# Kernel tuning notes

Measured on AMD Instinct MI355X. Metric: run time of the kernel, lower is better.

The kernel has to match this reference:

```python
import jax, jax.numpy as jnp
import numpy as np

E, D_IN, H1, H2 = 10, 784, 256, 64


def setup_inputs() -> dict:
    key = jax.random.key(0)
    ks = jax.random.split(key, 11)
    s = lambda fan_in: 1.0 / np.sqrt(fan_in)
    return {
        "x": jax.random.normal(ks[0], (65536, D_IN), dtype=jnp.float32),
        # stacked expert weights (E experts of Linear layers)
        "W1": jax.random.uniform(ks[1], (E, D_IN, H1), jnp.float32, -s(D_IN), s(D_IN)),
        "b1": jax.random.uniform(ks[2], (E, H1), jnp.float32, -s(D_IN), s(D_IN)),
        "W2": jax.random.uniform(ks[3], (E, H1, H2), jnp.float32, -s(H1), s(H1)),
        "b2": jax.random.uniform(ks[4], (E, H2), jnp.float32, -s(H1), s(H1)),
        "W3": jax.random.uniform(ks[5], (E, H2), jnp.float32, -s(H2), s(H2)),  # [E,64,1] squeezed
        "b3": jax.random.uniform(ks[6], (E,), jnp.float32, -s(H2), s(H2)),
        # gate: 784 -> 256 -> E
        "Wg1": jax.random.uniform(ks[7], (D_IN, H1), jnp.float32, -s(D_IN), s(D_IN)),
        "bg1": jax.random.uniform(ks[8], (H1,), jnp.float32, -s(D_IN), s(D_IN)),
        "Wg2": jax.random.uniform(ks[9], (H1, E), jnp.float32, -s(H1), s(H1)),
        "bg2": jax.random.uniform(ks[10], (E,), jnp.float32, -s(H1), s(H1)),
    }


def reference(x, W1, b1, W2, b2, W3, b3, Wg1, bg1, Wg2, bg2):
    # dense all-experts MLP stack, batched over experts as grouped GEMMs
    h = jax.nn.relu(jnp.einsum("bi,eih->beh", x, W1) + b1)        # [B,E,256]
    h = jax.nn.relu(jnp.einsum("beh,ehk->bek", h, W2) + b2)        # [B,E,64]
    expert_outputs = jnp.einsum("bek,ek->be", h, W3) + b3          # [B,E]
    g = jax.nn.relu(x @ Wg1 + bg1)
    gate_scores = jax.nn.softmax(g @ Wg2 + bg2, axis=-1)           # [B,E]
    output = gate_scores * expert_outputs                          # [B,E]
    return (output, gate_scores, expert_outputs)
```

## Files before the change

kernel.cpp:

```cpp
#include <hip/hip_runtime.h>
#include <hip/hip_bf16.h>
#include <stdint.h>

#define BTOT   65536
#define DIN    784
#define NH1    256
#define NH2    64
#define NEXP   10
#define BM     256
#define NKS1   25

#define SLOT(s)   (lds + (s) * 32768)
#define EXPL_OFF  131072
#define B2S_OFF   141312
#define W3S_OFF   143872
#define B3S_OFF   146432
#define BG2S_OFF  146496
#define LDS_TOTAL 146560

typedef short s16x8  __attribute__((ext_vector_type(8)));
typedef float f32x4  __attribute__((ext_vector_type(4)));
typedef float f32x16 __attribute__((ext_vector_type(16)));

__device__ __forceinline__ short bf16b(float v) {
    __bf16 b = (__bf16)v;
    return __builtin_bit_cast(short, b);
}

__device__ __forceinline__ void g2l16(const void* g, void* l) {
    __builtin_amdgcn_global_load_lds(
        (const __attribute__((address_space(1))) unsigned char*)g,
        (__attribute__((address_space(3))) unsigned char*)l, 16, 0, 0);
}

__global__ void prep_w1(const float* __restrict__ W1, const float* __restrict__ b1,
                        const float* __restrict__ Wg1, const float* __restrict__ bg1,
                        __bf16* __restrict__ dst) {
    int t = blockIdx.x * 256 + threadIdx.x;
    int lane = t & 63;
    int kh = (t >> 6) & 1;
    int nb = (t >> 7) & 7;
    int r  = t >> 10;
    int ks = r % 25, e = r / 25;
    int n  = nb * 32 + (lane & 31);
    int k0 = ks * 32 + kh * 16 + (lane >> 5) * 8;
    const float* src  = (e < NEXP) ? (W1 + (size_t)e * DIN * NH1) : Wg1;
    const float* bias = (e < NEXP) ? (b1 + e * NH1) : bg1;
    s16x8 o;
    #pragma unroll
    for (int j = 0; j < 8; ++j) {
        int k = k0 + j;
        float v = (k < DIN) ? src[(size_t)k * NH1 + n]
                            : ((k == DIN) ? bias[n] : 0.f);
        o[j] = bf16b(v);
    }
    *(s16x8*)((short*)dst + (size_t)t * 8) = o;
}

__global__ void prep_w2(const float* __restrict__ W2, __bf16* __restrict__ dst) {
    int t = blockIdx.x * 256 + threadIdx.x;
    int lane = t & 63;
    int kh = (t >> 6) & 1;
    int ks = (t >> 7) & 7;
    int jb = (t >> 10) & 1;
    int e  = t >> 11;
    int n  = jb * 32 + (lane & 31);
    int k0 = ks * 32 + kh * 16 + (lane >> 5) * 8;
    s16x8 o;
    #pragma unroll
    for (int j = 0; j < 8; ++j)
        o[j] = bf16b(W2[((size_t)e * NH1 + k0 + j) * NH2 + n]);
    *(s16x8*)((short*)dst + (size_t)t * 8) = o;
}

__global__ void prep_wg2(const float* __restrict__ Wg2, __bf16* __restrict__ dst) {
    int t = blockIdx.x * 256 + threadIdx.x;
    if (t >= 1024) return;
    int lane = t & 63;
    int kh = (t >> 6) & 1;
    int ks = t >> 7;
    int n  = lane & 31;
    int k0 = ks * 32 + kh * 16 + (lane >> 5) * 8;
    s16x8 o;
    #pragma unroll
    for (int j = 0; j < 8; ++j)
        o[j] = bf16b((n < NEXP) ? Wg2[(size_t)(k0 + j) * NEXP + n] : 0.f);
    *(s16x8*)((short*)dst + (size_t)t * 8) = o;
}

#define STAGE(S, E, KS) {                                                     \
        const char* xs_ = xtc + ((size_t)(KS) << 14) + tid * 16;              \
        char* xd_ = SLOT(S) + tid * 16;                                       \
        g2l16(xs_, xd_); g2l16(xs_ + 8192, xd_ + 8192);                       \
        const char* ws_ = w1c + (((size_t)(E) * 25 + (KS)) << 14) + tid * 16; \
        char* wd_ = SLOT(S) + 16384 + tid * 16;                               \
        g2l16(ws_, wd_); g2l16(ws_ + 8192, wd_ + 8192); }

#define WSTAGE1(S, KS) {                                                      \
        const char* ws_ = w1c + ((size_t)(KS) << 14) + tid * 16;              \
        char* wd_ = SLOT(S) + 16384 + tid * 16;                               \
        g2l16(ws_, wd_); g2l16(ws_ + 8192, wd_ + 8192); }

#define XLOAD(KS) { if ((KS) < 24 || xkh == 0) {                              \
            _Pragma("unroll") for (int i4 = 0; i4 < 4; ++i4)                  \
                *(float4*)(xf + 4 * i4) =                                     \
                    *(const float4*)(xrp + (KS) * 32 + 4 * i4);               \
        } else { _Pragma("unroll") for (int i4 = 0; i4 < 16; ++i4)            \
                     xf[i4] = 0.f;                                            \
                 xf[0] = 1.f; } }

#define XWRITE(B, KS) { s16x8 l8, h8;                                         \
        _Pragma("unroll") for (int j = 0; j < 8; ++j) {                       \
            l8[j] = bf16b(xf[j]); h8[j] = bf16b(xf[8 + j]); }                 \
        *(s16x8*)(SLOT(B) + xoff)       = l8;                                 \
        *(s16x8*)(SLOT(B) + xoff + 512) = h8;                                 \
        char* xg_ = xtw + ((size_t)(KS) << 14) + xoff;                        \
        *(s16x8*)xg_ = l8; *(s16x8*)(xg_ + 512) = h8; }

#define COMPUTE(S) {                                                          \
        const char* ab = SLOT(S) + mw * 4096 + lane * 16;                     \
        const char* wb = SLOT(S) + 16384 + nw * 8192 + lane * 16;             \
        s16x8 xv[2][2], wv[4][2];                                             \
        _Pragma("unroll") for (int mt = 0; mt < 2; ++mt)                      \
            _Pragma("unroll") for (int kh = 0; kh < 2; ++kh)                  \
                xv[mt][kh] = *(const s16x8*)(ab + (mt * 2 + kh) * 1024);      \
        _Pragma("unroll") for (int nt = 0; nt < 4; ++nt)                      \
            _Pragma("unroll") for (int kh = 0; kh < 2; ++kh)                  \
                wv[nt][kh] = *(const s16x8*)(wb + (nt * 2 + kh) * 1024);      \
        _Pragma("unroll") for (int kh = 0; kh < 2; ++kh)                      \
            _Pragma("unroll") for (int nt = 0; nt < 4; ++nt)                  \
                _Pragma("unroll") for (int mt = 0; mt < 2; ++mt)              \
                    acc[nt][mt] = __builtin_amdgcn_mfma_f32_32x32x16_bf16(    \
                        wv[nt][kh], xv[mt][kh], acc[nt][mt], 0, 0, 0); }

#define RING_SYNC(VN) {                                                       \
        asm volatile("s_waitcnt vmcnt(" #VN ")" ::: "memory");                \
        __builtin_amdgcn_s_barrier();                                         \
        asm volatile("" ::: "memory"); }

#define BODY(S, KS) {                                                         \
        RING_SYNC(8)                                                          \
        COMPUTE(S)                                                            \
        STAGE(((S) + 3) & 3, e, (KS) + 3) }

__global__ void __launch_bounds__(512)
__attribute__((amdgpu_waves_per_eu(2, 2)))
moe_fused(const float* __restrict__ x, __bf16* __restrict__ xt,
          const float* __restrict__ b2g, const float* __restrict__ W3,
          const float* __restrict__ b3, const float* __restrict__ bg2,
          const __bf16* __restrict__ w1t, const __bf16* __restrict__ w2t,
          const __bf16* __restrict__ wg2t, float* __restrict__ out)
{
    extern __shared__ char lds[];
    char*  hb   = lds;
    float* expl = (float*)(lds + EXPL_OFF);
    float* b2s  = (float*)(lds + B2S_OFF);
    float* w3s  = (float*)(lds + W3S_OFF);
    float* b3s  = (float*)(lds + B3S_OFF);
    float* bg2s = (float*)(lds + BG2S_OFF);

    const int tid  = threadIdx.x;
    const int lane = tid & 63;
    const int wave = tid >> 6;
    const int rl   = lane & 31;
    const int hi   = lane >> 5;
    const int mw   = wave >> 1;
    const int nw   = wave & 1;
    const int row0 = blockIdx.x * BM;
    const char* w1c = (const char*)w1t;
    const char* w2c = (const char*)w2t;
    const char* wgc = (const char*)wg2t;
    const char* xtc = (const char*)xt + ((size_t)blockIdx.x * 25 << 14);
    char*       xtw = (char*)xt + ((size_t)blockIdx.x * 25 << 14);

    const int xrow = tid >> 1, xkh = tid & 1;
    const float* xrp = x + (size_t)(row0 + xrow) * DIN + xkh * 16;
    const int xoff = ((xrow >> 5) * 2 + xkh) * 1024 + (xrow & 31) * 16;
    float xf[16];

    for (int i = tid; i < NEXP * NH2; i += 512) { b2s[i] = b2g[i]; w3s[i] = W3[i]; }
    if (tid < NEXP) { b3s[tid] = b3[tid]; bg2s[tid] = bg2[tid]; }
    __syncthreads();

    f32x16 acc[4][2];

    #pragma unroll 1
    for (int e = 0; e <= NEXP; ++e) {
        #pragma unroll
        for (int nt = 0; nt < 4; ++nt)
            #pragma unroll
            for (int mt = 0; mt < 2; ++mt)
                #pragma unroll
                for (int q = 0; q < 16; ++q) acc[nt][mt][q] = 0.f;

        if (e == 0) {
            int cur = 0;
            XLOAD(0)
            WSTAGE1(0, 0)
            XWRITE(0, 0)
            __syncthreads();
            #pragma unroll 1
            for (int ks = 0; ks < NKS1; ++ks) {
                if (ks < 24) { XLOAD(ks + 1) WSTAGE1(cur ^ 1, ks + 1) }
                COMPUTE(cur)
                if (ks < 24) XWRITE(cur ^ 1, ks + 1)
                __syncthreads();
                cur ^= 1;
            }
        } else {
            STAGE(0, e, 0)
            STAGE(1, e, 1)
            STAGE(2, e, 2)
            #pragma unroll 1
            for (int T = 0; T < 5; ++T) {
                const int k4 = 4 * T;
                BODY(0, k4)
                BODY(1, k4 + 1)
                BODY(2, k4 + 2)
                BODY(3, k4 + 3)
            }
            BODY(0, 20)
            BODY(1, 21)
            RING_SYNC(8)  COMPUTE(2)
            RING_SYNC(4)  COMPUTE(3)
            RING_SYNC(0)  COMPUTE(0)
            __syncthreads();
        }

        #pragma unroll
        for (int mt = 0; mt < 2; ++mt)
            #pragma unroll
            for (int nt = 0; nt < 4; ++nt)
                #pragma unroll
                for (int q = 0; q < 4; ++q) {
                    uint2 wvv; short* p = (short*)&wvv;
                    #pragma unroll
                    for (int r2 = 0; r2 < 4; ++r2)
                        p[r2] = bf16b(fmaxf(acc[nt][mt][q * 4 + r2], 0.f));
                    *(uint2*)(hb + (((mw * 2 + mt) * 8 + (nw * 4 + nt)) * 2
                                    + (q >> 1)) * 1024
                                 + (q & 1) * 512 + rl * 16 + hi * 8) = wvv;
                }
        __syncthreads();

        if (e < NEXP) {
            f32x16 acc2[2];
            #pragma unroll
            for (int q = 0; q < 16; ++q) { acc2[0][q] = 0.f; acc2[1][q] = 0.f; }
            #pragma unroll
            for (int jb = 0; jb < 2; ++jb)
                #pragma unroll
                for (int k2 = 0; k2 < 8; ++k2)
                    #pragma unroll
                    for (int kh = 0; kh < 2; ++kh) {
                        s16x8 hf = *(const s16x8*)(hb + ((wave * 8 + k2) * 2 + kh) * 1024
                                                   + lane * 16);
                        s16x8 wf = *(const s16x8*)(w2c
                            + ((((size_t)e * 2 + jb) * 8 + k2) * 2 + kh) * 1024
                            + lane * 16);
                        acc2[jb] = __builtin_amdgcn_mfma_f32_32x32x16_bf16(
                            wf, hf, acc2[jb], 0, 0, 0);
                    }
            float part = 0.f;
            #pragma unroll
            for (int jb = 0; jb < 2; ++jb)
                #pragma unroll
                for (int q = 0; q < 4; ++q) {
                    f32x4 b2v = *(const f32x4*)(b2s + e * NH2 + jb * 32 + 8 * q + 4 * hi);
                    f32x4 w3v = *(const f32x4*)(w3s + e * NH2 + jb * 32 + 8 * q + 4 * hi);
                    #pragma unroll
                    for (int r2 = 0; r2 < 4; ++r2)
                        part += fmaxf(acc2[jb][q * 4 + r2] + b2v[r2], 0.f) * w3v[r2];
                }
            part += __shfl_xor(part, 32, 64);
            if (hi == 0)
                expl[(wave * 32 + rl) * NEXP + e] = part + b3s[e];
        } else {
            f32x16 acc3;
            #pragma unroll
            for (int q = 0; q < 16; ++q) acc3[q] = 0.f;
            #pragma unroll
            for (int k2 = 0; k2 < 8; ++k2)
                #pragma unroll
                for (int kh = 0; kh < 2; ++kh) {
                    s16x8 hf = *(const s16x8*)(hb + ((wave * 8 + k2) * 2 + kh) * 1024
                                               + lane * 16);
                    s16x8 gf = *(const s16x8*)(wgc + (k2 * 2 + kh) * 1024 + lane * 16);
                    acc3 = __builtin_amdgcn_mfma_f32_32x32x16_bf16(
                        gf, hf, acc3, 0, 0, 0);
                }
            const int m = wave * 32 + rl;
            float lv[16], mx = -1e30f;
            #pragma unroll
            for (int q = 0; q < 4; ++q)
                #pragma unroll
                for (int r2 = 0; r2 < 4; ++r2) {
                    int j = r2 + 8 * q + 4 * hi;
                    int rg = q * 4 + r2;
                    lv[rg] = (j < NEXP) ? (acc3[rg] + bg2s[j]) : -1e30f;
                    mx = fmaxf(mx, lv[rg]);
                }
            mx = fmaxf(mx, __shfl_xor(mx, 32, 64));
            float s = 0.f, pv[16];
            #pragma unroll
            for (int rg = 0; rg < 16; ++rg) {
                pv[rg] = (lv[rg] > -1e29f) ? __expf(lv[rg] - mx) : 0.f;
                s += pv[rg];
            }
            s += __shfl_xor(s, 32, 64);
            const float inv = 1.f / s;
            #pragma unroll
            for (int q = 0; q < 4; ++q)
                #pragma unroll
                for (int r2 = 0; r2 < 4; ++r2) {
                    int j = r2 + 8 * q + 4 * hi;
                    if (j < NEXP) {
                        float g  = pv[q * 4 + r2] * inv;
                        float eo = expl[m * NEXP + j];
                        size_t o = (size_t)(row0 + m) * NEXP + j;
                        out[o] = g * eo;
                        out[(size_t)BTOT * NEXP + o] = g;
                        out[(size_t)2 * BTOT * NEXP + o] = eo;
                    }
                }
        }
        __syncthreads();
    }
}

extern "C" void kernel_launch(void* const* d_in, const int* in_sizes, int n_in,
                              void* d_out, int out_size, void* d_ws, size_t ws_size,
                              hipStream_t stream) {
    (void)in_sizes; (void)n_in; (void)out_size; (void)ws_size;
    const float* x   = (const float*)d_in[0];
    const float* W1  = (const float*)d_in[1];
    const float* b1  = (const float*)d_in[2];
    const float* W2  = (const float*)d_in[3];
    const float* b2  = (const float*)d_in[4];
    const float* W3  = (const float*)d_in[5];
    const float* b3  = (const float*)d_in[6];
    const float* Wg1 = (const float*)d_in[7];
    const float* bg1 = (const float*)d_in[8];
    const float* Wg2 = (const float*)d_in[9];
    const float* bg2 = (const float*)d_in[10];

    __bf16* w1t  = (__bf16*)d_ws;
    __bf16* w2t  = w1t + (size_t)11 * 25 * 8192;
    __bf16* wg2t = w2t + (size_t)20480 * 8;
    __bf16* xt   = wg2t + (size_t)1024 * 8;

    hipFuncSetAttribute((const void*)moe_fused,
                        hipFuncAttributeMaxDynamicSharedMemorySize, LDS_TOTAL);

    prep_w1<<<1100, 256, 0, stream>>>(W1, b1, Wg1, bg1, w1t);
    prep_w2<<<80, 256, 0, stream>>>(W2, w2t);
    prep_wg2<<<4, 256, 0, stream>>>(Wg2, wg2t);
    moe_fused<<<BTOT / BM, 512, LDS_TOTAL, stream>>>(
        x, xt, b2, W3, b3, bg2, w1t, w2t, wg2t, (float*)d_out);
}
```

Before: 329.1 us.

## Reorder ring body loads before staging and restructure expert-0 pipeline with manual waits

In the expert ring loop, LDS fragment reads now happen before the next global stage is issued, followed by a sched_barrier and raised wave priority around the MFMA block. This is meant to overlap global prefetch with matrix math and let MFMA-issuing waves win arbitration. The gate/expert-0 loop is unrolled by two with explicit vmcnt/lgkmcnt waits and raw s_barrier in place of __syncthreads, which reorders the X load, weight stage and X write. The handwritten wait counts must stay in step with the outstanding memory operations, and the reordered expert-0 loop may leave less global latency hidden.

```diff
diff --git a/kernel.cpp b/kernel.cpp
--- a/kernel.cpp
+++ b/kernel.cpp
@@ -140,8 +140,36 @@
 
 #define BODY(S, KS) {                                                         \
         RING_SYNC(8)                                                          \
-        COMPUTE(S)                                                            \
-        STAGE(((S) + 3) & 3, e, (KS) + 3) }
+        const char* ab = SLOT(S) + mw * 4096 + lane * 16;                     \
+        const char* wb = SLOT(S) + 16384 + nw * 8192 + lane * 16;             \
+        s16x8 xv[2][2], wv[4][2];                                             \
+        _Pragma("unroll") for (int mt = 0; mt < 2; ++mt)                      \
+            _Pragma("unroll") for (int kh = 0; kh < 2; ++kh)                  \
+                xv[mt][kh] = *(const s16x8*)(ab + (mt * 2 + kh) * 1024);      \
+        _Pragma("unroll") for (int nt = 0; nt < 4; ++nt)                      \
+            _Pragma("unroll") for (int kh = 0; kh < 2; ++kh)                  \
+                wv[nt][kh] = *(const s16x8*)(wb + (nt * 2 + kh) * 1024);      \
+        STAGE(((S) + 3) & 3, e, (KS) + 3)                                     \
+        __builtin_amdgcn_sched_barrier(0);                                    \
+        __builtin_amdgcn_s_setprio(1);                                        \
+        _Pragma("unroll") for (int kh = 0; kh < 2; ++kh)                      \
+            _Pragma("unroll") for (int nt = 0; nt < 4; ++nt)                  \
+                _Pragma("unroll") for (int mt = 0; mt < 2; ++mt)              \
+                    acc[nt][mt] = __builtin_amdgcn_mfma_f32_32x32x16_bf16(    \
+                        wv[nt][kh], xv[mt][kh], acc[nt][mt], 0, 0, 0);        \
+        __builtin_amdgcn_s_setprio(0); }
+
+#define E0BODY(CUR, KS) {                                                     \
+        asm volatile("s_waitcnt vmcnt(2)" ::: "memory");                      \
+        __builtin_amdgcn_s_barrier();                                         \
+        asm volatile("" ::: "memory");                                        \
+        COMPUTE(CUR)                                                          \
+        if ((KS) < 24) {                                                      \
+            XLOAD((KS) + 1)                                                   \
+            WSTAGE1((CUR) ^ 1, (KS) + 1)                                      \
+            XWRITE((CUR) ^ 1, (KS) + 1)                                       \
+        }                                                                     \
+        asm volatile("s_waitcnt lgkmcnt(0)" ::: "memory"); }
 
 __global__ void __launch_bounds__(512)
 __attribute__((amdgpu_waves_per_eu(2, 2)))
@@ -194,19 +222,20 @@
                 for (int q = 0; q < 16; ++q) acc[nt][mt][q] = 0.f;
 
         if (e == 0) {
-            int cur = 0;
             XLOAD(0)
             WSTAGE1(0, 0)
             XWRITE(0, 0)
+            asm volatile("s_waitcnt lgkmcnt(0)" ::: "memory");
+            #pragma unroll 1
+            for (int T = 0; T < 12; ++T) {
+                E0BODY(0, 2 * T)
+                E0BODY(1, 2 * T + 1)
+            }
+            asm volatile("s_waitcnt vmcnt(2)" ::: "memory");
+            __builtin_amdgcn_s_barrier();
+            asm volatile("" ::: "memory");
+            COMPUTE(0)
             __syncthreads();
-            #pragma unroll 1
-            for (int ks = 0; ks < NKS1; ++ks) {
-                if (ks < 24) { XLOAD(ks + 1) WSTAGE1(cur ^ 1, ks + 1) }
-                COMPUTE(cur)
-                if (ks < 24) XWRITE(cur ^ 1, ks + 1)
-                __syncthreads();
-                cur ^= 1;
-            }
         } else {
             STAGE(0, e, 0)
             STAGE(1, e, 1)
```

Measured after the change: 348.4 us. 1.06x slower.
